# Kernel tuning notes

Hardware: AMD Instinct MI355X
Metric: run time of the kernel (lower is better)

## Reference

```python
import jax, jax.numpy as jnp
import numpy as np

B = 2
N_PER = 100000
M_PER = 27648
C = 32
Z, Y, X = 21, 400, 352
MAX_RANGE = (2, 2, 2)
RADIUS = 8.0
NSAMPLE = 16
VS = np.array([0.2, 0.2, 0.4], np.float32)  # voxel size (x, y, z)


def setup_inputs() -> dict:
    key = jax.random.key(0)
    ks = jax.random.split(key, 6)
    N = B * N_PER
    M = B * M_PER
    space = jnp.array([X * VS[0], Y * VS[1], Z * VS[2]], jnp.float32)
    xyz = jax.random.uniform(ks[0], (N, 3), jnp.float32) * space
    zc = jax.random.randint(ks[1], (M,), 0, Z)
    yc = jax.random.randint(ks[2], (M,), 0, Y)
    xc = jax.random.randint(ks[3], (M,), 0, X)
    bq = jnp.repeat(jnp.arange(B, dtype=jnp.int32), M_PER)
    new_coords = jnp.stack([bq, zc, yc, xc], 1).astype(jnp.int32)
    new_xyz = jnp.stack([(xc + 0.5) * VS[0], (yc + 0.5) * VS[1], (zc + 0.5) * VS[2]], 1).astype(jnp.float32)
    features = jax.random.normal(ks[4], (N, C), jnp.float32)
    raw = jax.random.randint(ks[5], (B, Z, Y, X), -N_PER, N_PER)
    offs = (jnp.arange(B) * N_PER)[:, None, None, None]
    voxel2point_indices = jnp.where(raw < 0, -1, raw + offs).astype(jnp.int32)
    xyz_batch_cnt = jnp.full((B,), N_PER, jnp.int32)
    new_xyz_batch_cnt = jnp.full((B,), M_PER, jnp.int32)
    return dict(new_coords=new_coords, xyz=xyz, xyz_batch_cnt=xyz_batch_cnt,
                new_xyz=new_xyz, new_xyz_batch_cnt=new_xyz_batch_cnt,
                features=features, voxel2point_indices=voxel2point_indices)


def _voxel_query(xyz, new_xyz, new_coords, point_indices):
    """Vectorized equivalent of the CUDA voxel_query kernel.
    Returns (idx (M, nsample) int32 global point indices, empty_ball_mask (M,) bool)."""
    zr, yr, xr = MAX_RANGE
    _, Zg, Yg, Xg = point_indices.shape
    M = new_coords.shape[0]
    dz, dy, dx = jnp.meshgrid(jnp.arange(-zr, zr + 1), jnp.arange(-yr, yr + 1),
                              jnp.arange(-xr, xr + 1), indexing='ij')
    offs = jnp.stack([dz.ravel(), dy.ravel(), dx.ravel()], 1)  # (K,3) in CUDA loop order z,y,x
    nb = new_coords[:, None, 1:4] + offs[None]                 # (M,K,3) candidate voxels
    lim = jnp.array([Zg, Yg, Xg])
    inb = jnp.all((nb >= 0) & (nb < lim), -1)                  # (M,K) in-bounds
    nbc = jnp.clip(nb, 0, lim - 1)
    b = new_coords[:, 0]
    pidx = point_indices[b[:, None], nbc[..., 0], nbc[..., 1], nbc[..., 2]]  # (M,K)
    valid = inb & (pidx >= 0)
    pts = xyz[jnp.maximum(pidx, 0)]                            # (M,K,3)
    d2 = jnp.sum((pts - new_xyz[:, None, :]) ** 2, -1)
    valid = valid & (d2 < RADIUS * RADIUS)
    cnt = jnp.minimum(valid.sum(-1), NSAMPLE)                  # (M,)
    # assign each valid candidate its in-order slot; overflow/invalid go to dump column
    slot = jnp.cumsum(valid, -1) - 1
    slot = jnp.where(valid & (slot < NSAMPLE), slot, NSAMPLE)
    rows = jnp.arange(M)[:, None]
    idx = jnp.zeros((M, NSAMPLE + 1), jnp.int32).at[rows, slot].set(pidx)[:, :NSAMPLE]
    first = idx[:, 0]  # CUDA pre-fills all slots with first found index
    idx = jnp.where(jnp.arange(NSAMPLE)[None, :] < cnt[:, None], idx, first[:, None])
    empty = cnt == 0
    idx = jnp.where(empty[:, None], 0, idx)
    return idx, empty


def reference(new_coords, xyz, xyz_batch_cnt, new_xyz, new_xyz_batch_cnt, features, voxel2point_indices):
    idx, empty = _voxel_query(xyz, new_xyz, new_coords, voxel2point_indices)
    # global -> batch-relative (as in the torch loop), empty balls -> 0 of their batch
    xyz_offs = jnp.concatenate([jnp.zeros(1, jnp.int32), jnp.cumsum(xyz_batch_cnt)[:-1].astype(jnp.int32)])
    qb = new_coords[:, 0]
    idx_rel = jnp.where(empty[:, None], 0, idx - xyz_offs[qb][:, None])
    # grouping_operation (stack version): gather with batch offset added back
    gidx = idx_rel + xyz_offs[qb][:, None]                     # (M, nsample) global indices
    grouped_xyz = jnp.transpose(xyz[gidx], (0, 2, 1))          # (M, 3, nsample)
    grouped_features = jnp.transpose(features[gidx], (0, 2, 1))  # (M, C, nsample)
    return grouped_features, grouped_xyz, empty
```

## Files before the change

### kernel.cpp

```cpp
#include <hip/hip_runtime.h>


constexpr int ZG = 21;
constexpr int YG = 400;
constexpr int XG = 352;
constexpr int NS = 16;
constexpr int CF = 32;
constexpr float R2 = 64.0f;

typedef float v4f __attribute__((ext_vector_type(4)));

__global__ __launch_bounds__(256) void pad_xyz_kernel(
    const float* __restrict__ xyz, float4* __restrict__ xyz4, int N)
{
    const int i = blockIdx.x * 256 + threadIdx.x;
    if (i < N) {
        const float* p = xyz + (size_t)i * 3;
        xyz4[i] = make_float4(p[0], p[1], p[2], 0.0f);
    }
}

__global__ __launch_bounds__(256) void vqg_kernel(
    const int*    __restrict__ new_coords,
    const float4* __restrict__ xyz4,
    const int*    __restrict__ xyz_batch_cnt,
    const float*  __restrict__ new_xyz,
    const float*  __restrict__ features,
    const int*    __restrict__ v2p,
    float* __restrict__ out_feat,
    float* __restrict__ out_xyz,
    float* __restrict__ out_empty,
    int M)
{
    const int lane = threadIdx.x & 63;
    const int m    = (blockIdx.x * 256 + threadIdx.x) >> 6;
    if (m >= M) return;

    const int4 qc = *reinterpret_cast<const int4*>(new_coords + (size_t)m * 4);
    const int b = qc.x, zc = qc.y, yc = qc.z, xc = qc.w;
    const float qx = new_xyz[m * 3 + 0];
    const float qy = new_xyz[m * 3 + 1];
    const float qz = new_xyz[m * 3 + 2];
    int boff = 0;
    for (int i = 0; i < b; ++i) boff += xyz_batch_cnt[i];
    const int* __restrict__ gb = v2p + (size_t)b * (ZG * YG * XG);

    const int n0 = lane;
    const int n1 = 64 + lane;
    int pidx0 = -1, pidx1 = -1;
    {
        const int z = zc + (n0 / 25 - 2);
        const int y = yc + ((n0 / 5) % 5 - 2);
        const int x = xc + (n0 % 5 - 2);
        if ((unsigned)z < (unsigned)ZG && (unsigned)y < (unsigned)YG &&
            (unsigned)x < (unsigned)XG)
            pidx0 = gb[((size_t)z * YG + y) * XG + x];
    }
    if (n1 < 125) {
        const int z = zc + (n1 / 25 - 2);
        const int y = yc + ((n1 / 5) % 5 - 2);
        const int x = xc + (n1 % 5 - 2);
        if ((unsigned)z < (unsigned)ZG && (unsigned)y < (unsigned)YG &&
            (unsigned)x < (unsigned)XG)
            pidx1 = gb[((size_t)z * YG + y) * XG + x];
    }

    float p0x = 0, p0y = 0, p0z = 0, p1x = 0, p1y = 0, p1z = 0;
    if (pidx0 >= 0) {
        const float4 p = xyz4[pidx0];
        p0x = p.x; p0y = p.y; p0z = p.z;
    }
    if (pidx1 >= 0) {
        const float4 p = xyz4[pidx1];
        p1x = p.x; p1y = p.y; p1z = p.z;
    }

    bool v0 = false, v1 = false;
    if (pidx0 >= 0) {
        const float dx = p0x - qx, dy = p0y - qy, dz = p0z - qz;
        v0 = __fadd_rn(__fadd_rn(__fmul_rn(dx, dx), __fmul_rn(dy, dy)),
                       __fmul_rn(dz, dz)) < R2;
    }
    if (pidx1 >= 0) {
        const float dx = p1x - qx, dy = p1y - qy, dz = p1z - qz;
        v1 = __fadd_rn(__fadd_rn(__fmul_rn(dx, dx), __fmul_rn(dy, dy)),
                       __fmul_rn(dz, dz)) < R2;
    }

    const unsigned long long below = (1ull << lane) - 1ull;
    const unsigned long long bal0 = __ballot(v0);
    const unsigned long long bal1 = __ballot(v1);
    const int c0   = (int)__popcll(bal0);
    const int cnt  = c0 + (int)__popcll(bal1);
    const int pos0 = (int)__popcll(bal0 & below);
    const int pos1 = c0 + (int)__popcll(bal1 & below);

    const int junk  = (16 + (lane & 31)) << 2;
    const int addr0 = (v0 && pos0 < NS) ? (pos0 << 2) : junk;
    const int addr1 = (v1 && pos1 < NS) ? (pos1 << 2) : junk;
    const int perm0 = __builtin_amdgcn_ds_permute(addr0, pidx0);
    const int perm1 = __builtin_amdgcn_ds_permute(addr1, pidx1);

    const int sel   = (lane < c0) ? perm0 : perm1;
    const int first = __shfl(sel, 0);
    const int cnt16 = cnt < NS ? cnt : NS;
    const int gfin  = (cnt == 0) ? boff : (((lane & 15) < cnt16) ? sel : first);

    if (lane < 48) {
        const int s = lane & 15;
        const int d = lane >> 4;
        const int row = __shfl(gfin, s);
        const float val = reinterpret_cast<const float*>(xyz4 + row)[d];
        __builtin_nontemporal_store(val, out_xyz + (size_t)m * 48 + d * 16 + s);
    }
    if (lane == 0)
        __builtin_nontemporal_store(cnt == 0 ? 1.0f : 0.0f, out_empty + m);

    const int s0 = (lane & 3) << 2;
    const int r0 = __shfl(gfin, s0 + 0);
    const int r1 = __shfl(gfin, s0 + 1);
    const int r2 = __shfl(gfin, s0 + 2);
    const int r3 = __shfl(gfin, s0 + 3);
    float* __restrict__ of = out_feat + (size_t)m * (CF * NS);
    #pragma unroll
    for (int k = 0; k < 2; ++k) {
        const int c = k * 16 + (lane >> 2);
        v4f v;
        v[0] = features[(size_t)r0 * CF + c];
        v[1] = features[(size_t)r1 * CF + c];
        v[2] = features[(size_t)r2 * CF + c];
        v[3] = features[(size_t)r3 * CF + c];
        __builtin_nontemporal_store(
            v, reinterpret_cast<v4f*>(of + k * 256 + (lane << 2)));
    }
}

extern "C" void kernel_launch(void* const* d_in, const int* in_sizes, int n_in,
                              void* d_out, int out_size, void* d_ws, size_t ws_size,
                              hipStream_t stream) {
    const int*   new_coords    = (const int*)d_in[0];
    const float* xyz           = (const float*)d_in[1];
    const int*   xyz_batch_cnt = (const int*)d_in[2];
    const float* new_xyz       = (const float*)d_in[3];
    const float* features      = (const float*)d_in[5];
    const int*   v2p           = (const int*)d_in[6];

    const int M = in_sizes[0] / 4;
    const int N = in_sizes[1] / 3;

    float* out_feat  = (float*)d_out;
    float* out_xyz   = out_feat + (size_t)M * CF * NS;
    float* out_empty = out_xyz + (size_t)M * 3 * NS;

    float4* xyz4 = (float4*)d_ws;
    pad_xyz_kernel<<<(N + 255) / 256, 256, 0, stream>>>(xyz, xyz4, N);

    const int blocks = (M + 3) / 4;
    vqg_kernel<<<blocks, 256, 0, stream>>>(
        new_coords, xyz4, xyz_batch_cnt, new_xyz, features, v2p,
        out_feat, out_xyz, out_empty, M);
}
```

Before: 61.85 us.

## Sort queries by (batch,z,y) via counting sort and swizzle blocks across XCDs

```diff
diff --git a/kernel.cpp b/kernel.cpp
--- a/kernel.cpp
+++ b/kernel.cpp
@@ -18,6 +18,59 @@
         const float* p = xyz + (size_t)i * 3;
         xyz4[i] = make_float4(p[0], p[1], p[2], 0.0f);
     }
+}
+
+__global__ __launch_bounds__(256) void zero_kernel(int* __restrict__ p, int n)
+{
+    const int i = blockIdx.x * 256 + threadIdx.x;
+    if (i < n) p[i] = 0;
+}
+
+__global__ __launch_bounds__(256) void hist_kernel(
+    const int* __restrict__ nc, int* __restrict__ hist, int M)
+{
+    const int m = blockIdx.x * 256 + threadIdx.x;
+    if (m >= M) return;
+    const int4 qc = *reinterpret_cast<const int4*>(nc + (size_t)m * 4);
+    const int key = (qc.x * ZG + qc.y) * YG + qc.z;
+    atomicAdd(&hist[key], 1);
+}
+
+__global__ __launch_bounds__(1024) void scan_kernel(int* __restrict__ hist, int nbin)
+{
+    __shared__ int s[1024];
+    const int t = threadIdx.x;
+    const int chunk = (nbin + 1023) >> 10;
+    const int lo = t * chunk;
+    const int hi = min(lo + chunk, nbin);
+    int sum = 0;
+    for (int i = lo; i < hi; ++i) sum += hist[i];
+    s[t] = sum;
+    __syncthreads();
+    for (int off = 1; off < 1024; off <<= 1) {
+        const int u = (t >= off) ? s[t - off] : 0;
+        __syncthreads();
+        s[t] += u;
+        __syncthreads();
+    }
+    int run = s[t] - sum;
+    for (int i = lo; i < hi; ++i) {
+        const int c = hist[i];
+        hist[i] = run;
+        run += c;
+    }
+}
+
+__global__ __launch_bounds__(256) void scatter_kernel(
+    const int* __restrict__ nc, int* __restrict__ base,
+    int* __restrict__ qid, int M)
+{
+    const int m = blockIdx.x * 256 + threadIdx.x;
+    if (m >= M) return;
+    const int4 qc = *reinterpret_cast<const int4*>(nc + (size_t)m * 4);
+    const int key = (qc.x * ZG + qc.y) * YG + qc.z;
+    const int pos = atomicAdd(&base[key], 1);
+    qid[pos] = m;
 }
 
 __global__ __launch_bounds__(256) void vqg_kernel(
@@ -27,14 +80,20 @@
     const float*  __restrict__ new_xyz,
     const float*  __restrict__ features,
     const int*    __restrict__ v2p,
+    const int*    __restrict__ qid,
     float* __restrict__ out_feat,
     float* __restrict__ out_xyz,
     float* __restrict__ out_empty,
     int M)
 {
     const int lane = threadIdx.x & 63;
-    const int m    = (blockIdx.x * 256 + threadIdx.x) >> 6;
-    if (m >= M) return;
+    const int wid  = threadIdx.x >> 6;
+    const int nwg = gridDim.x;
+    int bid = blockIdx.x;
+    if ((nwg & 7) == 0) bid = (bid & 7) * (nwg >> 3) + (bid >> 3);
+    const int slot = bid * 4 + wid;
+    if (slot >= M) return;
+    const int m = qid[slot];
 
     const int4 qc = *reinterpret_cast<const int4*>(new_coords + (size_t)m * 4);
     const int b = qc.x, zc = qc.y, yc = qc.z, xc = qc.w;
@@ -147,16 +206,25 @@
 
     const int M = in_sizes[0] / 4;
     const int N = in_sizes[1] / 3;
+    const int B = in_sizes[2];
+    const int nbin = B * ZG * YG;
 
     float* out_feat  = (float*)d_out;
     float* out_xyz   = out_feat + (size_t)M * CF * NS;
     float* out_empty = out_xyz + (size_t)M * 3 * NS;
 
     float4* xyz4 = (float4*)d_ws;
+    int* hist = (int*)(xyz4 + N);
+    int* qid  = hist + nbin;
+
     pad_xyz_kernel<<<(N + 255) / 256, 256, 0, stream>>>(xyz, xyz4, N);
+    zero_kernel<<<(nbin + 255) / 256, 256, 0, stream>>>(hist, nbin);
+    hist_kernel<<<(M + 255) / 256, 256, 0, stream>>>(new_coords, hist, M);
+    scan_kernel<<<1, 1024, 0, stream>>>(hist, nbin);
+    scatter_kernel<<<(M + 255) / 256, 256, 0, stream>>>(new_coords, hist, qid, M);
 
     const int blocks = (M + 3) / 4;
     vqg_kernel<<<blocks, 256, 0, stream>>>(
-        new_coords, xyz4, xyz_batch_cnt, new_xyz, features, v2p,
+        new_coords, xyz4, xyz_batch_cnt, new_xyz, features, v2p, qid,
         out_feat, out_xyz, out_empty, M);
 }
```

Measured after the change: 83.77 us. 35.4% more time.
